# Kernel optimization log

Measured on AMD Instinct MI355X. Metric: run time of the kernel, lower is better.

The kernel has to match this reference:

```python
import jax, jax.numpy as jnp
import numpy as np

T, H, E, I, SI, TOP_K = 4096, 2048, 16, 1024, 4096, 1


def setup_inputs() -> dict:
    key = jax.random.key(0)
    ks = jax.random.split(key, 8)
    s_h = 1.0 / np.sqrt(H)
    s_i = 1.0 / np.sqrt(I)
    s_si = 1.0 / np.sqrt(SI)
    return {
        "hidden_states": jax.random.normal(ks[0], (T, H), jnp.float32),
        "router_w": jax.random.normal(ks[1], (E, H), jnp.float32) * s_h,
        "w_gate": jax.random.normal(ks[2], (E, H, I), jnp.float32) * s_h,
        "w_up": jax.random.normal(ks[3], (E, H, I), jnp.float32) * s_h,
        "w_down": jax.random.normal(ks[4], (E, I, H), jnp.float32) * s_i,
        "ws_gate": jax.random.normal(ks[5], (H, SI), jnp.float32) * s_h,
        "ws_up": jax.random.normal(ks[6], (H, SI), jnp.float32) * s_h,
        "ws_down": jax.random.normal(ks[7], (SI, H), jnp.float32) * s_si,
    }


def reference(hidden_states, router_w, w_gate, w_up, w_down, ws_gate, ws_up, ws_down):
    x = hidden_states  # [T, H]
    # Router: logits -> top-k -> sigmoid weights (Llama4RenormalizeMoeRoutingMethod)
    logits = jnp.einsum("th,eh->te", x, router_w)              # [T, E]
    top_vals, top_idx = jax.lax.top_k(logits, TOP_K)            # [T, K]
    weights = jax.nn.sigmoid(top_vals)                          # [T, K]
    # dispatch[t, e] = router weight if expert e selected for token t, else 0
    onehot = jax.nn.one_hot(top_idx, E, dtype=x.dtype)          # [T, K, E]
    dispatch = jnp.einsum("tke,tk->te", onehot, weights)        # [T, E]
    # Routed experts: router weight applied on input (commutes through the
    # linear gate/up projections as a per-(t,e) scalar applied before SiLU).
    g = jnp.einsum("th,ehi->tei", x, w_gate) * dispatch[:, :, None]  # [T, E, I]
    u = jnp.einsum("th,ehi->tei", x, w_up) * dispatch[:, :, None]    # [T, E, I]
    act = jax.nn.silu(g) * u                                          # [T, E, I]
    # Unselected experts contribute exactly 0 (act==0 there), so summing over
    # E in the down projection is the combine step.
    routed = jnp.einsum("tei,eih->th", act, w_down)             # [T, H]
    # Shared expert (SiLU-gated MLP on the unscaled hidden states)
    shared = (jax.nn.silu(x @ ws_gate) * (x @ ws_up)) @ ws_down  # [T, H]
    return shared + routed
```

## Files before the change

### kernel.cpp

```cpp
#include <hip/hip_runtime.h>
#include <hip/hip_bf16.h>

typedef unsigned short u16;
typedef unsigned int   u32;
typedef __attribute__((ext_vector_type(8))) short short8;
typedef __attribute__((ext_vector_type(4))) float f32x4;

#define T_TOK 4096
#define HDIM  2048
#define NEXP  16
#define IDIM  1024
#define SIDIM 4096
#define RCAP  6144
#define NTIL  48

#define O_WT      0u
#define O_EIDX    16384u
#define O_CNT     32768u
#define O_POS     32832u
#define O_PADOFF  32896u
#define O_TILEEXP 33024u
#define O_TOKROW  33280u
#define O_XBF     65536u
#define O_XSC     (O_XBF  + 2u*T_TOK*HDIM)
#define O_ACTS    (O_XSC  + 2u*RCAP*HDIM)
#define O_ACTR    (O_ACTS + 2u*T_TOK*SIDIM)
#define O_WSGT    (O_ACTR + 2u*RCAP*IDIM)
#define O_WSUT    (O_WSGT + 2u*SIDIM*HDIM)
#define O_WSDT    (O_WSUT + 2u*SIDIM*HDIM)
#define O_WGT     (O_WSDT + 2u*HDIM*SIDIM)
#define O_WUT     (O_WGT  + 2u*NEXP*IDIM*HDIM)
#define O_WDT     (O_WUT  + 2u*NEXP*IDIM*HDIM)

__device__ __forceinline__ u16 f2b(float f) {
  u32 u = __float_as_uint(f);
  u = (u + 0x7FFFu + ((u >> 16) & 1u)) >> 16;
  return (u16)u;
}

#define GLDS16(g, l) __builtin_amdgcn_global_load_lds( \
    (const __attribute__((address_space(1))) void*)(g), \
    (__attribute__((address_space(3))) void*)(l), 16, 0, 0)
#define BARX() __builtin_amdgcn_s_barrier()
#define SETPRIO(x) __builtin_amdgcn_s_setprio(x)
#define WAITVM(n) asm volatile("s_waitcnt vmcnt(" #n ")" ::: "memory")

__global__ __launch_bounds__(256) void router_k(
    const float* __restrict__ x, const float* __restrict__ rw,
    float* __restrict__ wt, int* __restrict__ eidx, int* __restrict__ cnt,
    u16* __restrict__ xbf) {
  int w = threadIdx.x >> 6, l = threadIdx.x & 63;
  int t = blockIdx.x * 4 + w;
  double acc[NEXP];
#pragma unroll
  for (int e = 0; e < NEXP; ++e) acc[e] = 0.0;
  const float* xp = x + (size_t)t * HDIM;
  u16* xo = xbf + (size_t)t * HDIM;
  for (int hb = 0; hb < HDIM; hb += 256) {
    float4 xv = *(const float4*)(xp + hb + l * 4);
    uint2 o;
    o.x = (u32)f2b(xv.x) | ((u32)f2b(xv.y) << 16);
    o.y = (u32)f2b(xv.z) | ((u32)f2b(xv.w) << 16);
    *(uint2*)(xo + hb + l * 4) = o;
#pragma unroll
    for (int e = 0; e < NEXP; ++e) {
      float4 wv = *(const float4*)(rw + (size_t)e * HDIM + hb + l * 4);
      acc[e] += (double)xv.x * wv.x + (double)xv.y * wv.y
              + (double)xv.z * wv.z + (double)xv.w * wv.w;
    }
  }
#pragma unroll
  for (int e = 0; e < NEXP; ++e) {
    double v = acc[e];
#pragma unroll
    for (int off = 32; off; off >>= 1) v += __shfl_xor(v, off, 64);
    acc[e] = v;
  }
  if (l == 0) {
    double best = acc[0]; int be = 0;
#pragma unroll
    for (int e = 1; e < NEXP; ++e) if (acc[e] > best) { best = acc[e]; be = e; }
    wt[t] = 1.0f / (1.0f + __expf(-(float)best));
    eidx[t] = be;
    atomicAdd(&cnt[be], 1);
  }
}

__global__ void scan_k(const int* __restrict__ cnt, int* __restrict__ pad_off,
                       int* __restrict__ tile_exp, int* __restrict__ pos,
                       int* __restrict__ tok_row) {
  if (threadIdx.x == 0) {
    for (int i = 0; i < 64; ++i) tile_exp[i] = -1;
    int run = 0;
    for (int e = 0; e < NEXP; ++e) {
      pad_off[e] = run;
      int pc = ((cnt[e] + 127) >> 7) << 7;
      for (int tt = run >> 7; tt < (run + pc) >> 7; ++tt) tile_exp[tt] = e;
      run += pc;
      pos[e] = 0;
    }
    pad_off[NEXP] = run;
  }
  for (int i = threadIdx.x; i < RCAP; i += 256) tok_row[i] = -1;
}

__global__ void assign_k(const int* __restrict__ eidx, const int* __restrict__ pad_off,
                         int* __restrict__ pos, int* __restrict__ tok_row) {
  int t = blockIdx.x * 256 + threadIdx.x;
  if (t >= T_TOK) return;
  int e = eidx[t];
  int r = atomicAdd(&pos[e], 1);
  tok_row[pad_off[e] + r] = t;
}

__global__ __launch_bounds__(256) void gather_k(
    const float* __restrict__ x, const float* __restrict__ wt,
    const int* __restrict__ tok_row, u16* __restrict__ xsc) {
  int g = blockIdx.x;
  int tid = threadIdx.x;
  u16* dst = xsc + (size_t)g * HDIM;
  int t = tok_row[g];
  if (t < 0) {
    uint2 z; z.x = 0u; z.y = 0u;
#pragma unroll
    for (int i = 0; i < 2; ++i) *(uint2*)(dst + i * 1024 + tid * 4) = z;
  } else {
    float s = wt[t];
    const float* src = x + (size_t)t * HDIM;
#pragma unroll
    for (int i = 0; i < 2; ++i) {
      int c = i * 1024 + tid * 4;
      float4 v = *(const float4*)(src + c);
      uint2 o;
      o.x = (u32)f2b(v.x * s) | ((u32)f2b(v.y * s) << 16);
      o.y = (u32)f2b(v.z * s) | ((u32)f2b(v.w * s) << 16);
      *(uint2*)(dst + c) = o;
    }
  }
}

__global__ __launch_bounds__(256) void tconv_k(
    const float* __restrict__ src, u16* __restrict__ dst, int K, int N) {
  __shared__ u32 lt[64][36];
  size_t boff = (size_t)blockIdx.z * (size_t)K * N;
  const int n0 = blockIdx.x * 64, k0 = blockIdx.y * 64;
  const int l = threadIdx.x & 63, w = threadIdx.x >> 6;
  const float* sp = src + boff + (size_t)(k0 + w * 16) * N + n0 + l;
  u32 p[8];
#pragma unroll
  for (int i = 0; i < 8; ++i) {
    float a = sp[(size_t)(2 * i) * N];
    float b = sp[(size_t)(2 * i + 1) * N];
    p[i] = (u32)f2b(a) | ((u32)f2b(b) << 16);
  }
  *(uint4*)&lt[l][w * 8 + 0] = make_uint4(p[0], p[1], p[2], p[3]);
  *(uint4*)&lt[l][w * 8 + 4] = make_uint4(p[4], p[5], p[6], p[7]);
  __syncthreads();
  const int c = threadIdx.x & 7, n2 = threadIdx.x >> 3;
#pragma unroll
  for (int rnd = 0; rnd < 2; ++rnd) {
    int n = n2 + rnd * 32;
    uint4 v = *(const uint4*)&lt[n][c * 4];
    *(uint4*)(dst + boff + (size_t)(n0 + n) * K + k0 + c * 8) = v;
  }
}


__device__ __forceinline__ void mmA(f32x4 (&acc)[4][8], const short8 (&af)[4],
                                    const short8 (&bfr)[4], int h) {
  SETPRIO(1);
#pragma unroll
  for (int mf = 0; mf < 4; ++mf)
#pragma unroll
    for (int nf = 0; nf < 4; ++nf)
      acc[mf][h * 4 + nf] = __builtin_amdgcn_mfma_f32_16x16x32_bf16(
          af[mf], bfr[nf], acc[mf][h * 4 + nf], 0, 0, 0);
  SETPRIO(0);
}
__device__ __forceinline__ void mmD(f32x4 (&acc)[4][4], const short8 (&af)[4],
                                    const short8 (&bfr)[2], int h) {
  SETPRIO(1);
#pragma unroll
  for (int mf = 0; mf < 4; ++mf)
#pragma unroll
    for (int nf = 0; nf < 2; ++nf)
      acc[mf][h * 2 + nf] = __builtin_amdgcn_mfma_f32_16x16x32_bf16(
          af[mf], bfr[nf], acc[mf][h * 2 + nf], 0, 0, 0);
  SETPRIO(0);
}

__global__ __launch_bounds__(512, 2) void gu_sh8(
    const u16* __restrict__ A, const u16* __restrict__ Bg, const u16* __restrict__ Bu,
    u16* __restrict__ act) {
  extern __shared__ u16 sm[];
  u16* As  = sm;
  u16* Bsm = sm + 32768;
  const int bid = blockIdx.x;
  const int swz = (bid & 7) * 64 + (bid >> 3);
  const int bx = swz & 31, by = swz >> 5;
  const int m0 = by * 256, c0 = bx * 128;
  const int tid = threadIdx.x, l = tid & 63, wid = tid >> 6;
  const int wm = wid >> 1, wn = wid & 1;

  const int cpos = tid & 3, rr = tid >> 2;
  const int gc = (cpos ^ ((rr >> 1) & 3)) * 8;
  const u16* aS0 = A + (size_t)(m0 + rr) * HDIM + gc;
  const u16* aS1 = A + (size_t)(m0 + 128 + rr) * HDIM + gc;
  const int mat = (rr >> 6) & 1;
  const u16* bbase = mat ? Bu : Bg;
  const u16* bS0 = bbase + (size_t)(c0 + (rr & 63)) * HDIM + gc;
  const u16* bS1 = bbase + (size_t)(c0 + 64 + (rr & 63)) * HDIM + gc;
  const int ld0 = tid * 8, ld1 = (512 + tid) * 8;

#define STA_G(bb, kh, koff) do { \
    GLDS16(aS0 + (koff) + (kh) * 32, As + ((bb) * 2 + (kh)) * 8192 + ld0); \
    GLDS16(aS1 + (koff) + (kh) * 32, As + ((bb) * 2 + (kh)) * 8192 + ld1); } while (0)
#define STB_G(bb, kh, koff) do { \
    GLDS16(bS0 + (koff) + (kh) * 32, Bsm + ((bb) * 2 + (kh)) * 8192 + ld0); \
    GLDS16(bS1 + (koff) + (kh) * 32, Bsm + ((bb) * 2 + (kh)) * 8192 + ld1); } while (0)

  const int fch = ((l >> 4) ^ ((l >> 1) & 3)) * 8;
  int aoff[4], boff[8];
#pragma unroll
  for (int mf = 0; mf < 4; ++mf) aoff[mf] = (wm * 64 + mf * 16 + (l & 15)) * 32 + fch;
#pragma unroll
  for (int i = 0; i < 8; ++i) {
    int v = wn * 128 + (i >> 2) * 64 + (i & 3) * 16 + (l & 15);
    boff[i] = v * 32 + fch;
  }
#define LDA_G(bb, kh) do { const u16* s_ = As + ((bb) * 2 + (kh)) * 8192; \
    af[0] = *(const short8*)(s_ + aoff[0]); af[1] = *(const short8*)(s_ + aoff[1]); \
    af[2] = *(const short8*)(s_ + aoff[2]); af[3] = *(const short8*)(s_ + aoff[3]); } while (0)
#define LDB_G(bb, kh, h) do { const u16* s_ = Bsm + ((bb) * 2 + (kh)) * 8192; \
    bfr[0] = *(const short8*)(s_ + boff[(h) * 4 + 0]); bfr[1] = *(const short8*)(s_ + boff[(h) * 4 + 1]); \
    bfr[2] = *(const short8*)(s_ + boff[(h) * 4 + 2]); bfr[3] = *(const short8*)(s_ + boff[(h) * 4 + 3]); } while (0)

  f32x4 acc[4][8];
#pragma unroll
  for (int i = 0; i < 4; ++i)
#pragma unroll
    for (int j = 0; j < 8; ++j)
#pragma unroll
      for (int r = 0; r < 4; ++r) acc[i][j][r] = 0.0f;
  short8 af[4], bfr[4];

  STA_G(0, 0, 0); STB_G(0, 0, 0); STA_G(0, 1, 0); STB_G(0, 1, 0);
  WAITVM(0); BARX();
  const int NT = HDIM / 64;
  for (int t = 0; t < NT - 1; ++t) {
    const int b = t & 1, nb = b ^ 1, kn = (t + 1) * 64;
    LDA_G(b, 0); LDB_G(b, 0, 0); STA_G(nb, 0, kn); BARX(); mmA(acc, af, bfr, 0); BARX();
    LDB_G(b, 0, 1);              STB_G(nb, 0, kn); BARX(); mmA(acc, af, bfr, 1); WAITVM(4); BARX();
    LDA_G(b, 1); LDB_G(b, 1, 0); STA_G(nb, 1, kn); BARX(); mmA(acc, af, bfr, 0); BARX();
    LDB_G(b, 1, 1);              STB_G(nb, 1, kn); BARX(); mmA(acc, af, bfr, 1); WAITVM(4); BARX();
  }
  { const int b = (NT - 1) & 1;
    LDA_G(b, 0); LDB_G(b, 0, 0); BARX(); mmA(acc, af, bfr, 0); BARX();
    LDB_G(b, 0, 1);              BARX(); mmA(acc, af, bfr, 1); WAITVM(0); BARX();
    LDA_G(b, 1); LDB_G(b, 1, 0); BARX(); mmA(acc, af, bfr, 0); BARX();
    LDB_G(b, 1, 1);              mmA(acc, af, bfr, 1);
  }
#pragma unroll
  for (int mf = 0; mf < 4; ++mf)
#pragma unroll
    for (int nf = 0; nf < 4; ++nf) {
      int col = c0 + wn * 64 + nf * 16 + (l & 15);
      int rowb = m0 + wm * 64 + mf * 16 + (l >> 4) * 4;
#pragma unroll
      for (int r = 0; r < 4; ++r) {
        float g = acc[mf][nf][r], u = acc[mf][4 + nf][r];
        float s = g / (1.0f + __expf(-g));
        act[(size_t)(rowb + r) * SIDIM + col] = f2b(s * u);
      }
    }
#undef STA_G
#undef STB_G
#undef LDA_G
#undef LDB_G
}

__global__ __launch_bounds__(512, 2) void dn_sh8(
    const u16* __restrict__ A, const u16* __restrict__ B, float* __restrict__ out) {
  extern __shared__ u16 sm[];
  u16* As  = sm;
  u16* Bsm = sm + 32768;
  const int bid = blockIdx.x;
  const int swz = (bid & 7) * 32 + (bid >> 3);
  const int bx = swz & 15, by = swz >> 4;
  const int m0 = by * 256, c0 = bx * 128;
  const int tid = threadIdx.x, l = tid & 63, wid = tid >> 6;
  const int wm = wid >> 1, wn = wid & 1;

  const int cpos = tid & 3, rr = tid >> 2;
  const int gc = (cpos ^ ((rr >> 1) & 3)) * 8;
  const u16* aS0 = A + (size_t)(m0 + rr) * SIDIM + gc;
  const u16* aS1 = A + (size_t)(m0 + 128 + rr) * SIDIM + gc;
  const u16* bS  = B + (size_t)(c0 + rr) * SIDIM + gc;
  const int ld0 = tid * 8, ld1 = (512 + tid) * 8;

#define STA_D(bb, kh, koff) do { \
    GLDS16(aS0 + (koff) + (kh) * 32, As + ((bb) * 2 + (kh)) * 8192 + ld0); \
    GLDS16(aS1 + (koff) + (kh) * 32, As + ((bb) * 2 + (kh)) * 8192 + ld1); } while (0)
#define STB_D(bb, kh, koff) \
    GLDS16(bS + (koff) + (kh) * 32, Bsm + ((bb) * 2 + (kh)) * 4096 + ld0)

  const int fch = ((l >> 4) ^ ((l >> 1) & 3)) * 8;
  int aoff[4], boff[4];
#pragma unroll
  for (int mf = 0; mf < 4; ++mf) aoff[mf] = (wm * 64 + mf * 16 + (l & 15)) * 32 + fch;
#pragma unroll
  for (int i = 0; i < 4; ++i) {
    int v = wn * 64 + (i >> 1) * 32 + (i & 1) * 16 + (l & 15);
    boff[i] = v * 32 + fch;
  }
#define LDA_D(bb, kh) do { const u16* s_ = As + ((bb) * 2 + (kh)) * 8192; \
    af[0] = *(const short8*)(s_ + aoff[0]); af[1] = *(const short8*)(s_ + aoff[1]); \
    af[2] = *(const short8*)(s_ + aoff[2]); af[3] = *(const short8*)(s_ + aoff[3]); } while (0)
#define LDB_D(bb, kh, h) do { const u16* s_ = Bsm + ((bb) * 2 + (kh)) * 4096; \
    bfr[0] = *(const short8*)(s_ + boff[(h) * 2 + 0]); \
    bfr[1] = *(const short8*)(s_ + boff[(h) * 2 + 1]); } while (0)

  f32x4 acc[4][4];
#pragma unroll
  for (int i = 0; i < 4; ++i)
#pragma unroll
    for (int j = 0; j < 4; ++j)
#pragma unroll
      for (int r = 0; r < 4; ++r) acc[i][j][r] = 0.0f;
  short8 af[4]; short8 bfr[2];

  STA_D(0, 0, 0); STB_D(0, 0, 0); STA_D(0, 1, 0); STB_D(0, 1, 0);
  WAITVM(0); BARX();
  const int NT = SIDIM / 64;
  for (int t = 0; t < NT - 1; ++t) {
    const int b = t & 1, nb = b ^ 1, kn = (t + 1) * 64;
    LDA_D(b, 0); LDB_D(b, 0, 0); STA_D(nb, 0, kn); BARX(); mmD(acc, af, bfr, 0); BARX();
    LDB_D(b, 0, 1);              STB_D(nb, 0, kn); BARX(); mmD(acc, af, bfr, 1); WAITVM(3); BARX();
    LDA_D(b, 1); LDB_D(b, 1, 0); STA_D(nb, 1, kn); BARX(); mmD(acc, af, bfr, 0); BARX();
    LDB_D(b, 1, 1);              STB_D(nb, 1, kn); BARX(); mmD(acc, af, bfr, 1); WAITVM(3); BARX();
  }
  { const int b = (NT - 1) & 1;
    LDA_D(b, 0); LDB_D(b, 0, 0); BARX(); mmD(acc, af, bfr, 0); BARX();
    LDB_D(b, 0, 1);              BARX(); mmD(acc, af, bfr, 1); WAITVM(0); BARX();
    LDA_D(b, 1); LDB_D(b, 1, 0); BARX(); mmD(acc, af, bfr, 0); BARX();
    LDB_D(b, 1, 1);              mmD(acc, af, bfr, 1);
  }
#pragma unroll
  for (int mf = 0; mf < 4; ++mf)
#pragma unroll
    for (int nf = 0; nf < 4; ++nf) {
      int col = c0 + wn * 64 + (nf >> 1) * 32 + (nf & 1) * 16 + (l & 15);
      int rowb = m0 + wm * 64 + mf * 16 + (l >> 4) * 4;
#pragma unroll
      for (int r = 0; r < 4; ++r)
        out[(size_t)(rowb + r) * HDIM + col] = acc[mf][nf][r];
    }
#undef STA_D
#undef STB_D
#undef LDA_D
#undef LDB_D
}

__global__ __launch_bounds__(256) void gu_r(
    const u16* __restrict__ A, const u16* __restrict__ BgT, const u16* __restrict__ BuT,
    u16* __restrict__ act, const int* __restrict__ tile_exp) {
  __shared__ __align__(16) u16 As[128 * 64];
  __shared__ __align__(16) u16 Bgs[64 * 64];
  __shared__ __align__(16) u16 Bus[64 * 64];
  const int tid = threadIdx.x;
  const int l = tid & 63, w = tid >> 6;
  const int wm = w >> 1, wn = w & 1;
  const int m0 = blockIdx.y * 128, n0 = blockIdx.x * 64;
  int e = tile_exp[blockIdx.y];
  if (e < 0) return;
  size_t eo = (size_t)e * IDIM * HDIM;
  const u16* Bg = BgT + eo + (size_t)n0 * HDIM;
  const u16* Bu = BuT + eo + (size_t)n0 * HDIM;
  f32x4 accg[4][2], accu[4][2];
#pragma unroll
  for (int i = 0; i < 4; ++i)
#pragma unroll
    for (int j = 0; j < 2; ++j)
#pragma unroll
      for (int r = 0; r < 4; ++r) { accg[i][j][r] = 0.0f; accu[i][j][r] = 0.0f; }
  const u16* Ab = A + (size_t)m0 * HDIM;

  for (int k0 = 0; k0 < HDIM; k0 += 64) {
    __syncthreads();
#pragma unroll
    for (int j = 0; j < 4; ++j) {
      int c = j * 256 + tid, r = c >> 3, cc = c & 7;
      GLDS16(Ab + (size_t)r * HDIM + k0 + ((cc ^ (r & 7)) * 8), &As[c * 8]);
    }
#pragma unroll
    for (int j = 0; j < 2; ++j) {
      int c = j * 256 + tid, r = c >> 3, cc = c & 7;
      int sc = (cc ^ (r & 7)) * 8;
      GLDS16(Bg + (size_t)r * HDIM + k0 + sc, &Bgs[c * 8]);
      GLDS16(Bu + (size_t)r * HDIM + k0 + sc, &Bus[c * 8]);
    }
    __syncthreads();
#pragma unroll
    for (int kh = 0; kh < 2; ++kh) {
      const int q = kh * 4 + (l >> 4);
      short8 af[4];
#pragma unroll
      for (int mf = 0; mf < 4; ++mf) {
        int r = wm * 64 + mf * 16 + (l & 15);
        af[mf] = *(const short8*)&As[r * 64 + ((q ^ (r & 7)) * 8)];
      }
      short8 bgf[2], buf2[2];
#pragma unroll
      for (int nf = 0; nf < 2; ++nf) {
        int n = wn * 32 + nf * 16 + (l & 15);
        bgf[nf]  = *(const short8*)&Bgs[n * 64 + ((q ^ (n & 7)) * 8)];
        buf2[nf] = *(const short8*)&Bus[n * 64 + ((q ^ (n & 7)) * 8)];
      }
#pragma unroll
      for (int mf = 0; mf < 4; ++mf)
#pragma unroll
        for (int nf = 0; nf < 2; ++nf) {
          accg[mf][nf] = __builtin_amdgcn_mfma_f32_16x16x32_bf16(af[mf], bgf[nf],  accg[mf][nf], 0, 0, 0);
          accu[mf][nf] = __builtin_amdgcn_mfma_f32_16x16x32_bf16(af[mf], buf2[nf], accu[mf][nf], 0, 0, 0);
        }
    }
  }
#pragma unroll
  for (int mf = 0; mf < 4; ++mf)
#pragma unroll
    for (int nf = 0; nf < 2; ++nf) {
      int col = n0 + wn * 32 + nf * 16 + (l & 15);
#pragma unroll
      for (int r = 0; r < 4; ++r) {
        int row = m0 + wm * 64 + mf * 16 + (l >> 4) * 4 + r;
        float g = accg[mf][nf][r], u = accu[mf][nf][r];
        float s = g / (1.0f + __expf(-g));
        act[(size_t)row * IDIM + col] = f2b(s * u);
      }
    }
}

__global__ __launch_bounds__(256) void dn_r(
    const u16* __restrict__ A, const u16* __restrict__ BT, float* __restrict__ out,
    const int* __restrict__ tile_exp, const int* __restrict__ tok_row) {
  __shared__ __align__(16) u16 As[128 * 64];
  __shared__ __align__(16) u16 Bs[128 * 64];
  const int tid = threadIdx.x;
  const int l = tid & 63, w = tid >> 6;
  const int wm = w >> 1, wn = w & 1;
  const int m0 = blockIdx.y * 128, n0 = blockIdx.x * 128;
  int e = tile_exp[blockIdx.y];
  if (e < 0) return;
  const u16* B = BT + (size_t)e * HDIM * IDIM + (size_t)n0 * IDIM;
  f32x4 acc[4][4];
#pragma unroll
  for (int i = 0; i < 4; ++i)
#pragma unroll
    for (int j = 0; j < 4; ++j)
#pragma unroll
      for (int r = 0; r < 4; ++r) acc[i][j][r] = 0.0f;
  const u16* Ab = A + (size_t)m0 * IDIM;

  for (int k0 = 0; k0 < IDIM; k0 += 64) {
    __syncthreads();
#pragma unroll
    for (int j = 0; j < 4; ++j) {
      int c = j * 256 + tid, r = c >> 3, cc = c & 7;
      GLDS16(Ab + (size_t)r * IDIM + k0 + ((cc ^ (r & 7)) * 8), &As[c * 8]);
    }
#pragma unroll
    for (int j = 0; j < 4; ++j) {
      int c = j * 256 + tid, r = c >> 3, cc = c & 7;
      GLDS16(B + (size_t)r * IDIM + k0 + ((cc ^ (r & 7)) * 8), &Bs[c * 8]);
    }
    __syncthreads();
#pragma unroll
    for (int kh = 0; kh < 2; ++kh) {
      const int q = kh * 4 + (l >> 4);
      short8 af[4];
#pragma unroll
      for (int mf = 0; mf < 4; ++mf) {
        int r = wm * 64 + mf * 16 + (l & 15);
        af[mf] = *(const short8*)&As[r * 64 + ((q ^ (r & 7)) * 8)];
      }
      short8 bf[4];
#pragma unroll
      for (int nf = 0; nf < 4; ++nf) {
        int n = wn * 64 + nf * 16 + (l & 15);
        bf[nf] = *(const short8*)&Bs[n * 64 + ((q ^ (n & 7)) * 8)];
      }
#pragma unroll
      for (int mf = 0; mf < 4; ++mf)
#pragma unroll
        for (int nf = 0; nf < 4; ++nf)
          acc[mf][nf] = __builtin_amdgcn_mfma_f32_16x16x32_bf16(af[mf], bf[nf], acc[mf][nf], 0, 0, 0);
    }
  }
#pragma unroll
  for (int mf = 0; mf < 4; ++mf)
#pragma unroll
    for (int nf = 0; nf < 4; ++nf) {
      int col = n0 + wn * 64 + nf * 16 + (l & 15);
#pragma unroll
      for (int r = 0; r < 4; ++r) {
        int grow = m0 + wm * 64 + mf * 16 + (l >> 4) * 4 + r;
        int t = tok_row[grow];
        if (t >= 0) out[(size_t)t * HDIM + col] += acc[mf][nf][r];
      }
    }
}

extern "C" void kernel_launch(void* const* d_in, const int* in_sizes, int n_in,
                              void* d_out, int out_size, void* d_ws, size_t ws_size,
                              hipStream_t stream) {
  const float* x   = (const float*)d_in[0];
  const float* rw  = (const float*)d_in[1];
  const float* wg  = (const float*)d_in[2];
  const float* wu  = (const float*)d_in[3];
  const float* wd  = (const float*)d_in[4];
  const float* wsg = (const float*)d_in[5];
  const float* wsu = (const float*)d_in[6];
  const float* wsd = (const float*)d_in[7];
  float* out = (float*)d_out;
  char* ws = (char*)d_ws;

  float* wt     = (float*)(ws + O_WT);
  int* eidx     = (int*)(ws + O_EIDX);
  int* cnt      = (int*)(ws + O_CNT);
  int* pos      = (int*)(ws + O_POS);
  int* pad_off  = (int*)(ws + O_PADOFF);
  int* tile_exp = (int*)(ws + O_TILEEXP);
  int* tok_row  = (int*)(ws + O_TOKROW);
  u16* xbf      = (u16*)(ws + O_XBF);
  u16* xsc      = (u16*)(ws + O_XSC);
  u16* acts     = (u16*)(ws + O_ACTS);
  u16* actr     = (u16*)(ws + O_ACTR);
  u16* wsgT     = (u16*)(ws + O_WSGT);
  u16* wsuT     = (u16*)(ws + O_WSUT);
  u16* wsdT     = (u16*)(ws + O_WSDT);
  u16* wgT      = (u16*)(ws + O_WGT);
  u16* wuT      = (u16*)(ws + O_WUT);
  u16* wdT      = (u16*)(ws + O_WDT);

  hipFuncSetAttribute((const void*)gu_sh8, hipFuncAttributeMaxDynamicSharedMemorySize, 131072);
  hipFuncSetAttribute((const void*)dn_sh8, hipFuncAttributeMaxDynamicSharedMemorySize, 98304);

  hipMemsetAsync(ws + O_CNT, 0, 128, stream);
  tconv_k<<<dim3(SIDIM / 64, HDIM / 64, 1), 256, 0, stream>>>(wsg, wsgT, HDIM, SIDIM);
  tconv_k<<<dim3(SIDIM / 64, HDIM / 64, 1), 256, 0, stream>>>(wsu, wsuT, HDIM, SIDIM);
  tconv_k<<<dim3(HDIM / 64, SIDIM / 64, 1), 256, 0, stream>>>(wsd, wsdT, SIDIM, HDIM);
  tconv_k<<<dim3(IDIM / 64, HDIM / 64, NEXP), 256, 0, stream>>>(wg, wgT, HDIM, IDIM);
  tconv_k<<<dim3(IDIM / 64, HDIM / 64, NEXP), 256, 0, stream>>>(wu, wuT, HDIM, IDIM);
  tconv_k<<<dim3(HDIM / 64, IDIM / 64, NEXP), 256, 0, stream>>>(wd, wdT, IDIM, HDIM);

  router_k<<<T_TOK / 4, 256, 0, stream>>>(x, rw, wt, eidx, cnt, xbf);
  scan_k<<<1, 256, 0, stream>>>(cnt, pad_off, tile_exp, pos, tok_row);
  assign_k<<<T_TOK / 256, 256, 0, stream>>>(eidx, pad_off, pos, tok_row);
  gather_k<<<RCAP, 256, 0, stream>>>(x, wt, tok_row, xsc);

  gu_sh8<<<512, 512, 131072, stream>>>(xbf, wsgT, wsuT, acts);
  gu_r<<<dim3(IDIM / 64, NTIL), 256, 0, stream>>>(xsc, wgT, wuT, actr, tile_exp);
  dn_sh8<<<256, 512, 98304, stream>>>(acts, wsdT, out);
  dn_r<<<dim3(HDIM / 128, NTIL), 256, 0, stream>>>(actr, wdT, out, tile_exp, tok_row);
}
```

Before: 672.4 us.

## Merge weight conversion kernels, rework XCD swizzle and batch MFMA phases in shared GEMMs

Replaces the six per-weight transpose/convert launches with one flat-indexed kernel covering all weights, removing several launch gaps. The shared-expert gate/up and down GEMMs get a new block-to-XCD mapping so neighbouring column tiles land on the same XCD. Both GEMMs now load both B-fragment halves before one larger MFMA burst, halving the barriers per k-step. They also relax the prologue wait count. The extra fragment registers may raise register pressure, and the relaxed initial wait could be a correctness risk.

```diff
diff --git a/kernel.cpp b/kernel.cpp
--- a/kernel.cpp
+++ b/kernel.cpp
@@ -139,13 +139,12 @@
   }
 }
 
-__global__ __launch_bounds__(256) void tconv_k(
-    const float* __restrict__ src, u16* __restrict__ dst, int K, int N) {
-  __shared__ u32 lt[64][36];
-  size_t boff = (size_t)blockIdx.z * (size_t)K * N;
-  const int n0 = blockIdx.x * 64, k0 = blockIdx.y * 64;
-  const int l = threadIdx.x & 63, w = threadIdx.x >> 6;
-  const float* sp = src + boff + (size_t)(k0 + w * 16) * N + n0 + l;
+__device__ __forceinline__ void conv_tile(
+    const float* __restrict__ src, u16* __restrict__ dst, int K, int N,
+    int bx, int ky, u32 (*lt)[36], int tid) {
+  const int n0 = bx * 64, k0 = ky * 64;
+  const int l = tid & 63, w = tid >> 6;
+  const float* sp = src + (size_t)(k0 + w * 16) * N + n0 + l;
   u32 p[8];
 #pragma unroll
   for (int i = 0; i < 8; ++i) {
@@ -156,38 +155,43 @@
   *(uint4*)&lt[l][w * 8 + 0] = make_uint4(p[0], p[1], p[2], p[3]);
   *(uint4*)&lt[l][w * 8 + 4] = make_uint4(p[4], p[5], p[6], p[7]);
   __syncthreads();
-  const int c = threadIdx.x & 7, n2 = threadIdx.x >> 3;
+  const int c = tid & 7, n2 = tid >> 3;
 #pragma unroll
   for (int rnd = 0; rnd < 2; ++rnd) {
     int n = n2 + rnd * 32;
     uint4 v = *(const uint4*)&lt[n][c * 4];
-    *(uint4*)(dst + boff + (size_t)(n0 + n) * K + k0 + c * 8) = v;
-  }
-}
-
-
-__device__ __forceinline__ void mmA(f32x4 (&acc)[4][8], const short8 (&af)[4],
-                                    const short8 (&bfr)[4], int h) {
-  SETPRIO(1);
-#pragma unroll
-  for (int mf = 0; mf < 4; ++mf)
-#pragma unroll
-    for (int nf = 0; nf < 4; ++nf)
-      acc[mf][h * 4 + nf] = __builtin_amdgcn_mfma_f32_16x16x32_bf16(
-          af[mf], bfr[nf], acc[mf][h * 4 + nf], 0, 0, 0);
-  SETPRIO(0);
-}
-__device__ __forceinline__ void mmD(f32x4 (&acc)[4][4], const short8 (&af)[4],
-                                    const short8 (&bfr)[2], int h) {
-  SETPRIO(1);
-#pragma unroll
-  for (int mf = 0; mf < 4; ++mf)
-#pragma unroll
-    for (int nf = 0; nf < 2; ++nf)
-      acc[mf][h * 2 + nf] = __builtin_amdgcn_mfma_f32_16x16x32_bf16(
-          af[mf], bfr[nf], acc[mf][h * 2 + nf], 0, 0, 0);
-  SETPRIO(0);
-}
+    *(uint4*)(dst + (size_t)(n0 + n) * K + k0 + c * 8) = v;
+  }
+}
+
+__global__ __launch_bounds__(256) void megaconv(
+    const float* __restrict__ wsg, const float* __restrict__ wsu,
+    const float* __restrict__ wsd, const float* __restrict__ wg,
+    const float* __restrict__ wu, const float* __restrict__ wd,
+    u16* wsgT, u16* wsuT, u16* wsdT, u16* wgT, u16* wuT, u16* wdT) {
+  __shared__ u32 lt[64][36];
+  int idx = blockIdx.x, tid = threadIdx.x;
+  if (idx < 2048) {
+    conv_tile(wsg, wsgT, 2048, 4096, idx & 63, idx >> 6, lt, tid);
+  } else if (idx < 4096) { idx -= 2048;
+    conv_tile(wsu, wsuT, 2048, 4096, idx & 63, idx >> 6, lt, tid);
+  } else if (idx < 12288) { idx -= 4096;
+    int e = idx >> 9, r = idx & 511;
+    conv_tile(wg + (size_t)e * HDIM * IDIM, wgT + (size_t)e * IDIM * HDIM,
+              2048, 1024, r & 15, r >> 4, lt, tid);
+  } else if (idx < 20480) { idx -= 12288;
+    int e = idx >> 9, r = idx & 511;
+    conv_tile(wu + (size_t)e * HDIM * IDIM, wuT + (size_t)e * IDIM * HDIM,
+              2048, 1024, r & 15, r >> 4, lt, tid);
+  } else if (idx < 22528) { idx -= 20480;
+    conv_tile(wsd, wsdT, 4096, 2048, idx & 31, idx >> 5, lt, tid);
+  } else { idx -= 22528;
+    int e = idx >> 9, r = idx & 511;
+    conv_tile(wd + (size_t)e * IDIM * HDIM, wdT + (size_t)e * HDIM * IDIM,
+              1024, 2048, r & 31, r >> 5, lt, tid);
+  }
+}
+
 
 __global__ __launch_bounds__(512, 2) void gu_sh8(
     const u16* __restrict__ A, const u16* __restrict__ Bg, const u16* __restrict__ Bu,
@@ -196,8 +200,8 @@
   u16* As  = sm;
   u16* Bsm = sm + 32768;
   const int bid = blockIdx.x;
-  const int swz = (bid & 7) * 64 + (bid >> 3);
-  const int bx = swz & 31, by = swz >> 5;
+  const int xcd = bid & 7, bi = bid >> 3;
+  const int bx = xcd * 4 + (bi & 3), by = bi >> 2;
   const int m0 = by * 256, c0 = bx * 128;
   const int tid = threadIdx.x, l = tid & 63, wid = tid >> 6;
   const int wm = wid >> 1, wn = wid & 1;
@@ -231,9 +235,16 @@
 #define LDA_G(bb, kh) do { const u16* s_ = As + ((bb) * 2 + (kh)) * 8192; \
     af[0] = *(const short8*)(s_ + aoff[0]); af[1] = *(const short8*)(s_ + aoff[1]); \
     af[2] = *(const short8*)(s_ + aoff[2]); af[3] = *(const short8*)(s_ + aoff[3]); } while (0)
-#define LDB_G(bb, kh, h) do { const u16* s_ = Bsm + ((bb) * 2 + (kh)) * 8192; \
-    bfr[0] = *(const short8*)(s_ + boff[(h) * 4 + 0]); bfr[1] = *(const short8*)(s_ + boff[(h) * 4 + 1]); \
-    bfr[2] = *(const short8*)(s_ + boff[(h) * 4 + 2]); bfr[3] = *(const short8*)(s_ + boff[(h) * 4 + 3]); } while (0)
+#define LDB_G(bb, kh, h, d) do { const u16* s_ = Bsm + ((bb) * 2 + (kh)) * 8192; \
+    d[0] = *(const short8*)(s_ + boff[(h) * 4 + 0]); d[1] = *(const short8*)(s_ + boff[(h) * 4 + 1]); \
+    d[2] = *(const short8*)(s_ + boff[(h) * 4 + 2]); d[3] = *(const short8*)(s_ + boff[(h) * 4 + 3]); } while (0)
+#define MM32_G() do { SETPRIO(1); \
+    _Pragma("unroll") for (int mf = 0; mf < 4; ++mf) { \
+      _Pragma("unroll") for (int nf = 0; nf < 4; ++nf) \
+        acc[mf][nf] = __builtin_amdgcn_mfma_f32_16x16x32_bf16(af[mf], bfrA[nf], acc[mf][nf], 0, 0, 0); \
+      _Pragma("unroll") for (int nf = 0; nf < 4; ++nf) \
+        acc[mf][4 + nf] = __builtin_amdgcn_mfma_f32_16x16x32_bf16(af[mf], bfrB[nf], acc[mf][4 + nf], 0, 0, 0); \
+    } SETPRIO(0); } while (0)
 
   f32x4 acc[4][8];
 #pragma unroll
@@ -242,23 +253,25 @@
     for (int j = 0; j < 8; ++j)
 #pragma unroll
       for (int r = 0; r < 4; ++r) acc[i][j][r] = 0.0f;
-  short8 af[4], bfr[4];
+  short8 af[4], bfrA[4], bfrB[4];
 
   STA_G(0, 0, 0); STB_G(0, 0, 0); STA_G(0, 1, 0); STB_G(0, 1, 0);
-  WAITVM(0); BARX();
+  WAITVM(4); BARX();
   const int NT = HDIM / 64;
   for (int t = 0; t < NT - 1; ++t) {
     const int b = t & 1, nb = b ^ 1, kn = (t + 1) * 64;
-    LDA_G(b, 0); LDB_G(b, 0, 0); STA_G(nb, 0, kn); BARX(); mmA(acc, af, bfr, 0); BARX();
-    LDB_G(b, 0, 1);              STB_G(nb, 0, kn); BARX(); mmA(acc, af, bfr, 1); WAITVM(4); BARX();
-    LDA_G(b, 1); LDB_G(b, 1, 0); STA_G(nb, 1, kn); BARX(); mmA(acc, af, bfr, 0); BARX();
-    LDB_G(b, 1, 1);              STB_G(nb, 1, kn); BARX(); mmA(acc, af, bfr, 1); WAITVM(4); BARX();
+    LDA_G(b, 0); LDB_G(b, 0, 0, bfrA); LDB_G(b, 0, 1, bfrB);
+    STA_G(nb, 0, kn); STB_G(nb, 0, kn);
+    BARX(); MM32_G(); WAITVM(4); BARX();
+    LDA_G(b, 1); LDB_G(b, 1, 0, bfrA); LDB_G(b, 1, 1, bfrB);
+    STA_G(nb, 1, kn); STB_G(nb, 1, kn);
+    BARX(); MM32_G(); WAITVM(4); BARX();
   }
   { const int b = (NT - 1) & 1;
-    LDA_G(b, 0); LDB_G(b, 0, 0); BARX(); mmA(acc, af, bfr, 0); BARX();
-    LDB_G(b, 0, 1);              BARX(); mmA(acc, af, bfr, 1); WAITVM(0); BARX();
-    LDA_G(b, 1); LDB_G(b, 1, 0); BARX(); mmA(acc, af, bfr, 0); BARX();
-    LDB_G(b, 1, 1);              mmA(acc, af, bfr, 1);
+    LDA_G(b, 0); LDB_G(b, 0, 0, bfrA); LDB_G(b, 0, 1, bfrB);
+    BARX(); MM32_G(); WAITVM(0); BARX();
+    LDA_G(b, 1); LDB_G(b, 1, 0, bfrA); LDB_G(b, 1, 1, bfrB);
+    MM32_G();
   }
 #pragma unroll
   for (int mf = 0; mf < 4; ++mf)
@@ -277,6 +290,7 @@
 #undef STB_G
 #undef LDA_G
 #undef LDB_G
+#undef MM32_G
 }
 
 __global__ __launch_bounds__(512, 2) void dn_sh8(
@@ -285,8 +299,8 @@
   u16* As  = sm;
   u16* Bsm = sm + 32768;
   const int bid = blockIdx.x;
-  const int swz = (bid & 7) * 32 + (bid >> 3);
-  const int bx = swz & 15, by = swz >> 4;
+  const int xcd = bid & 7, bi = bid >> 3;
+  const int bx = xcd * 2 + (bi & 1), by = bi >> 1;
   const int m0 = by * 256, c0 = bx * 128;
   const int tid = threadIdx.x, l = tid & 63, wid = tid >> 6;
   const int wm = wid >> 1, wn = wid & 1;
@@ -316,9 +330,16 @@
 #define LDA_D(bb, kh) do { const u16* s_ = As + ((bb) * 2 + (kh)) * 8192; \
     af[0] = *(const short8*)(s_ + aoff[0]); af[1] = *(const short8*)(s_ + aoff[1]); \
     af[2] = *(const short8*)(s_ + aoff[2]); af[3] = *(const short8*)(s_ + aoff[3]); } while (0)
-#define LDB_D(bb, kh, h) do { const u16* s_ = Bsm + ((bb) * 2 + (kh)) * 4096; \
-    bfr[0] = *(const short8*)(s_ + boff[(h) * 2 + 0]); \
-    bfr[1] = *(const short8*)(s_ + boff[(h) * 2 + 1]); } while (0)
+#define LDB_D(bb, kh, h, d) do { const u16* s_ = Bsm + ((bb) * 2 + (kh)) * 4096; \
+    d[0] = *(const short8*)(s_ + boff[(h) * 2 + 0]); \
+    d[1] = *(const short8*)(s_ + boff[(h) * 2 + 1]); } while (0)
+#define MM16_D() do { SETPRIO(1); \
+    _Pragma("unroll") for (int mf = 0; mf < 4; ++mf) { \
+      acc[mf][0] = __builtin_amdgcn_mfma_f32_16x16x32_bf16(af[mf], bfrA[0], acc[mf][0], 0, 0, 0); \
+      acc[mf][1] = __builtin_amdgcn_mfma_f32_16x16x32_bf16(af[mf], bfrA[1], acc[mf][1], 0, 0, 0); \
+      acc[mf][2] = __builtin_amdgcn_mfma_f32_16x16x32_bf16(af[mf], bfrB[0], acc[mf][2], 0, 0, 0); \
+      acc[mf][3] = __builtin_amdgcn_mfma_f32_16x16x32_bf16(af[mf], bfrB[1], acc[mf][3], 0, 0, 0); \
+    } SETPRIO(0); } while (0)
 
   f32x4 acc[4][4];
 #pragma unroll
@@ -327,23 +348,25 @@
     for (int j = 0; j < 4; ++j)
 #pragma unroll
       for (int r = 0; r < 4; ++r) acc[i][j][r] = 0.0f;
-  short8 af[4]; short8 bfr[2];
+  short8 af[4], bfrA[2], bfrB[2];
 
   STA_D(0, 0, 0); STB_D(0, 0, 0); STA_D(0, 1, 0); STB_D(0, 1, 0);
-  WAITVM(0); BARX();
+  WAITVM(3); BARX();
   const int NT = SIDIM / 64;
   for (int t = 0; t < NT - 1; ++t) {
     const int b = t & 1, nb = b ^ 1, kn = (t + 1) * 64;
-    LDA_D(b, 0); LDB_D(b, 0, 0); STA_D(nb, 0, kn); BARX(); mmD(acc, af, bfr, 0); BARX();
-    LDB_D(b, 0, 1);              STB_D(nb, 0, kn); BARX(); mmD(acc, af, bfr, 1); WAITVM(3); BARX();
-    LDA_D(b, 1); LDB_D(b, 1, 0); STA_D(nb, 1, kn); BARX(); mmD(acc, af, bfr, 0); BARX();
-    LDB_D(b, 1, 1);              STB_D(nb, 1, kn); BARX(); mmD(acc, af, bfr, 1); WAITVM(3); BARX();
+    LDA_D(b, 0); LDB_D(b, 0, 0, bfrA); LDB_D(b, 0, 1, bfrB);
+    STA_D(nb, 0, kn); STB_D(nb, 0, kn);
+    BARX(); MM16_D(); WAITVM(3); BARX();
+    LDA_D(b, 1); LDB_D(b, 1, 0, bfrA); LDB_D(b, 1, 1, bfrB);
+    STA_D(nb, 1, kn); STB_D(nb, 1, kn);
+    BARX(); MM16_D(); WAITVM(3); BARX();
   }
   { const int b = (NT - 1) & 1;
-    LDA_D(b, 0); LDB_D(b, 0, 0); BARX(); mmD(acc, af, bfr, 0); BARX();
-    LDB_D(b, 0, 1);              BARX(); mmD(acc, af, bfr, 1); WAITVM(0); BARX();
-    LDA_D(b, 1); LDB_D(b, 1, 0); BARX(); mmD(acc, af, bfr, 0); BARX();
-    LDB_D(b, 1, 1);              mmD(acc, af, bfr, 1);
+    LDA_D(b, 0); LDB_D(b, 0, 0, bfrA); LDB_D(b, 0, 1, bfrB);
+    BARX(); MM16_D(); WAITVM(0); BARX();
+    LDA_D(b, 1); LDB_D(b, 1, 0, bfrA); LDB_D(b, 1, 1, bfrB);
+    MM16_D();
   }
 #pragma unroll
   for (int mf = 0; mf < 4; ++mf)
@@ -359,6 +382,7 @@
 #undef STB_D
 #undef LDA_D
 #undef LDB_D
+#undef MM16_D
 }
 
 __global__ __launch_bounds__(256) void gu_r(
@@ -546,17 +570,12 @@
   hipFuncSetAttribute((const void*)dn_sh8, hipFuncAttributeMaxDynamicSharedMemorySize, 98304);
 
   hipMemsetAsync(ws + O_CNT, 0, 128, stream);
-  tconv_k<<<dim3(SIDIM / 64, HDIM / 64, 1), 256, 0, stream>>>(wsg, wsgT, HDIM, SIDIM);
-  tconv_k<<<dim3(SIDIM / 64, HDIM / 64, 1), 256, 0, stream>>>(wsu, wsuT, HDIM, SIDIM);
-  tconv_k<<<dim3(HDIM / 64, SIDIM / 64, 1), 256, 0, stream>>>(wsd, wsdT, SIDIM, HDIM);
-  tconv_k<<<dim3(IDIM / 64, HDIM / 64, NEXP), 256, 0, stream>>>(wg, wgT, HDIM, IDIM);
-  tconv_k<<<dim3(IDIM / 64, HDIM / 64, NEXP), 256, 0, stream>>>(wu, wuT, HDIM, IDIM);
-  tconv_k<<<dim3(HDIM / 64, IDIM / 64, NEXP), 256, 0, stream>>>(wd, wdT, IDIM, HDIM);
-
   router_k<<<T_TOK / 4, 256, 0, stream>>>(x, rw, wt, eidx, cnt, xbf);
   scan_k<<<1, 256, 0, stream>>>(cnt, pad_off, tile_exp, pos, tok_row);
   assign_k<<<T_TOK / 256, 256, 0, stream>>>(eidx, pad_off, pos, tok_row);
   gather_k<<<RCAP, 256, 0, stream>>>(x, wt, tok_row, xsc);
+  megaconv<<<30720, 256, 0, stream>>>(wsg, wsu, wsd, wg, wu, wd,
+                                      wsgT, wsuT, wsdT, wgT, wuT, wdT);
 
   gu_sh8<<<512, 512, 131072, stream>>>(xbf, wsgT, wsuT, acts);
   gu_r<<<dim3(IDIM / 64, NTIL), 256, 0, stream>>>(xsc, wgT, wuT, actr, tile_exp);
```

After: 667.7 us. About the same (-0.7%).
